# Kernel optimization log

Measured on AMD Instinct MI355X. Metric: run time of the kernel, lower is better.

## Reference

```python
import jax, jax.numpy as jnp
import numpy as np

NUM_PERS = 16
D = 128
N = 4096
EPSILON = 0.1
EPS_NORM = 1e-12  # matches torch F.normalize default eps


def setup_inputs() -> dict:
    key = jax.random.key(0)
    k1, k2 = jax.random.split(key)
    context = jax.random.normal(k1, (N, D), dtype=jnp.float32)
    # xavier_uniform for shape (num_pers, input_size): bound = sqrt(6/(fan_in+fan_out))
    bound = float(np.sqrt(6.0 / (NUM_PERS + D)))
    weight_tensor = jax.random.uniform(k2, (NUM_PERS, D), dtype=jnp.float32,
                                       minval=-bound, maxval=bound)
    return {"context": context, "weight_tensor": weight_tensor}


def reference(context, weight_tensor):
    # context: [N, D]; weight_tensor: [P, D]
    # per-perspective weighted features: [P, N, D]
    context_fc = context[None, :, :] * weight_tensor[:, None, :]
    # L2 normalize along feature dim (torch F.normalize: x / max(||x||, eps))
    norm = jnp.maximum(jnp.linalg.norm(context_fc, axis=-1, keepdims=True), EPS_NORM)
    context_norm = context_fc / norm
    # cosine similarity per perspective, mean over perspectives: [N, N]
    attention = jnp.einsum('pnd,pmd->pnm', context_norm, context_norm).mean(0)
    # epsilon neighbourhood with markoff_value = 0
    mask = (attention > EPSILON).astype(attention.dtype)
    return attention * mask
```

## Files before the change

kernel.cpp:

```cpp
#include <hip/hip_runtime.h>
#include <math.h>

#define N 4096
#define D 128
#define P 16
#define KK 2048
#define NT 32
#define NBLK (NT * (NT + 1) / 2)
#define LCAP 2048
#define CAP (1u << 20)
#define WIN 1.5e-3f
#define ZSCALE 256.0f
#define OSCALE (1.0f / 16777216.0f * 16.0f)

typedef _Float16 half_t;
typedef __attribute__((ext_vector_type(8))) _Float16 f16x8;
typedef __attribute__((ext_vector_type(4))) float f32x4;
typedef __attribute__((address_space(1))) const unsigned int* gptr_t;
typedef __attribute__((address_space(3))) unsigned int* lptr_t;

__global__ __launch_bounds__(256) void k_pack(const float* __restrict__ c,
                                              const float* __restrict__ w,
                                              double* __restrict__ rnorm,
                                              half_t* __restrict__ zb,
                                              unsigned* gcnt, unsigned* govf,
                                              int do_init) {
    int n = blockIdx.x, tid = threadIdx.x;
    if (do_init && n == 0 && tid == 0) { *gcnt = 0; *govf = 0; }
    int p = tid >> 4, d0 = (tid & 15) * 8;
    const float* cc = c + (size_t)n * D + d0;
    const float* ww = w + (size_t)p * D + d0;
    float cv[8], wv[8];
    *(float4*)&cv[0] = *(const float4*)&cc[0];
    *(float4*)&cv[4] = *(const float4*)&cc[4];
    *(float4*)&wv[0] = *(const float4*)&ww[0];
    *(float4*)&wv[4] = *(const float4*)&ww[4];
    double s = 0.0;
#pragma unroll
    for (int i = 0; i < 8; ++i) {
        double v = (double)cv[i] * (double)wv[i];
        s += v * v;
    }
#pragma unroll
    for (int o = 1; o < 16; o <<= 1) s += __shfl_xor(s, o, 64);
    double rn = 1.0 / fmax(sqrt(s), 1e-12);
    if ((tid & 15) == 0) rnorm[p * N + n] = rn;
    float rnf = (float)rn;
    f16x8 o8;
#pragma unroll
    for (int i = 0; i < 8; ++i) o8[i] = (half_t)(cv[i] * wv[i] * rnf * ZSCALE);
    *(f16x8*)&zb[(size_t)n * KK + tid * 8] = o8;
}

template <bool FUSED>
__global__ __launch_bounds__(256, 4) void k_gemm(const half_t* __restrict__ zb,
                                                 float* __restrict__ out,
                                                 unsigned* __restrict__ gcnt,
                                                 unsigned* __restrict__ govf,
                                                 unsigned* __restrict__ glist) {
    __shared__ __align__(16) half_t As[2][128 * 32];
    __shared__ __align__(16) half_t Bs[2][128 * 32];
    __shared__ unsigned lds_list[LCAP];
    __shared__ unsigned lds_cnt, lds_base, lds_tot;

    int tid = threadIdx.x;
    if (FUSED && tid == 0) lds_cnt = 0;

    int lane = tid & 63, wv = tid >> 6;
    int wr = wv >> 1, wc = wv & 1;

    int braw = blockIdx.x;
    int b = (braw & 7) * (NBLK / 8) + (braw >> 3);
    int ti = 0;
    while (b >= NT - ti) { b -= NT - ti; ++ti; }
    int tj = ti + b;
    int n0 = ti * 128, m0 = tj * 128;

    f32x4 acc[4][4] = {};
    int lrow = lane >> 2;
    int lchunk = (((lane & 3) ^ ((lrow >> 1) & 3)) * 8);

    auto STAGE = [&](int buf, int k0) {
#pragma unroll
        for (int h = 0; h < 2; ++h) {
            int s = h * 4 + wv;
            int row = s * 16 + lrow;
            __builtin_amdgcn_global_load_lds(
                (gptr_t)(zb + (size_t)(n0 + row) * KK + k0 + lchunk),
                (lptr_t)(&As[buf][s * 512]), 16, 0, 0);
            __builtin_amdgcn_global_load_lds(
                (gptr_t)(zb + (size_t)(m0 + row) * KK + k0 + lchunk),
                (lptr_t)(&Bs[buf][s * 512]), 16, 0, 0);
        }
    };

    int kk_c = lane >> 4;
    int rsel = lane & 15;
    int kphys = (kk_c ^ ((rsel >> 1) & 3)) * 8;

    auto COMPUTE = [&](int cur) {
        f16x8 af[4], bfr[4];
#pragma unroll
        for (int f = 0; f < 4; ++f) {
            af[f]  = *(f16x8*)&As[cur][(wr * 64 + f * 16 + rsel) * 32 + kphys];
            bfr[f] = *(f16x8*)&Bs[cur][(wc * 64 + f * 16 + rsel) * 32 + kphys];
        }
#pragma unroll
        for (int i = 0; i < 4; ++i)
#pragma unroll
            for (int j = 0; j < 4; ++j)
                acc[i][j] = __builtin_amdgcn_mfma_f32_16x16x32_f16(af[i], bfr[j], acc[i][j], 0, 0, 0);
    };

    STAGE(0, 0);

#pragma unroll 2
    for (int t = 0; t < 63; ++t) {
        int cur = t & 1;
        STAGE(cur ^ 1, (t + 1) * 32);
        asm volatile("s_waitcnt vmcnt(4)" ::: "memory");
        __builtin_amdgcn_sched_barrier(0);
        __builtin_amdgcn_s_barrier();
        __builtin_amdgcn_sched_barrier(0);
        COMPUTE(cur);
        asm volatile("s_waitcnt lgkmcnt(0)" ::: "memory");
        __builtin_amdgcn_sched_barrier(0);
        __builtin_amdgcn_s_barrier();
        __builtin_amdgcn_sched_barrier(0);
    }
    asm volatile("s_waitcnt vmcnt(0)" ::: "memory");
    __builtin_amdgcn_sched_barrier(0);
    __builtin_amdgcn_s_barrier();
    __builtin_amdgcn_sched_barrier(0);
    COMPUTE(1);

    int colD = lane & 15, rq = lane >> 4;
    bool mir = (ti != tj);
#pragma unroll
    for (int i = 0; i < 4; ++i)
#pragma unroll
        for (int j = 0; j < 4; ++j) {
            int rbase = n0 + wr * 64 + i * 16 + rq * 4;
            int ccol = m0 + wc * 64 + j * 16 + colD;
            float4 mv;
#pragma unroll
            for (int q = 0; q < 4; ++q) {
                float a = acc[i][j][q] * OSCALE;
                float sv;
                if (FUSED) {
                    bool flg = fabsf(a - 0.1f) < WIN;
                    sv = flg ? a : (a > 0.1f ? a : 0.0f);
                    if (flg) {
                        unsigned pos = atomicAdd(&lds_cnt, 1u);
                        unsigned ent = (unsigned)(rbase + q) | ((unsigned)ccol << 12) |
                                       (mir ? (1u << 24) : 0u);
                        if (pos < LCAP) lds_list[pos] = ent;
                    }
                } else {
                    sv = a;
                }
                out[(size_t)(rbase + q) * N + ccol] = sv;
                ((float*)&mv)[q] = sv;
            }
            if (mir) *(float4*)&out[(size_t)ccol * N + rbase] = mv;
        }

    if (FUSED) {
        __syncthreads();
        if (tid == 0) {
            unsigned tot = lds_cnt;
            unsigned cnt = tot > LCAP ? LCAP : tot;
            lds_tot = cnt;
            lds_base = atomicAdd(gcnt, cnt);
            if (tot > LCAP) atomicOr(govf, 1u);
        }
        __syncthreads();
        unsigned cnt = lds_tot, base = lds_base;
        for (unsigned e = tid; e < cnt; e += 256) {
            unsigned gi = base + e;
            if (gi < CAP) glist[gi] = lds_list[e];
            else atomicOr(govf, 1u);
        }
    }
}

__global__ __launch_bounds__(256) void k_fix3(const float* __restrict__ c,
                                              const float* __restrict__ w,
                                              const double* __restrict__ rnorm,
                                              const unsigned* __restrict__ gcnt,
                                              const unsigned* __restrict__ govf,
                                              const unsigned* __restrict__ glist,
                                              float* __restrict__ out) {
    __shared__ double w2[D * P];
    for (int e = threadIdx.x; e < P * D; e += 256) {
        int p = e >> 7, d = e & 127;
        double wv = (double)w[p * D + d];
        w2[d * P + p] = wv * wv;
    }
    __syncthreads();

    if (*govf) {
        size_t stride = (size_t)gridDim.x * 256;
        for (size_t idx = (size_t)blockIdx.x * 256 + threadIdx.x; idx < (size_t)N * N;
             idx += stride) {
            float a = out[idx];
            if (fabsf(a - 0.1f) >= WIN) {
                out[idx] = (a > 0.1f) ? a : 0.0f;
                continue;
            }
            int n = (int)(idx >> 12), m = (int)(idx & (N - 1));
            const float* cn = c + (size_t)n * D;
            const float* cm = c + (size_t)m * D;
            double acc[P];
#pragma unroll
            for (int p = 0; p < P; ++p) acc[p] = 0.0;
            for (int d0 = 0; d0 < D; d0 += 4) {
                float4 a4 = *(const float4*)&cn[d0];
                float4 b4 = *(const float4*)&cm[d0];
                float av[4] = {a4.x, a4.y, a4.z, a4.w};
                float bv[4] = {b4.x, b4.y, b4.z, b4.w};
#pragma unroll
                for (int q = 0; q < 4; ++q) {
                    double pr = (double)av[q] * (double)bv[q];
#pragma unroll
                    for (int p = 0; p < P; ++p) acc[p] += pr * w2[(d0 + q) * P + p];
                }
            }
            double t = 0.0;
#pragma unroll
            for (int p = 0; p < P; ++p)
                t += acc[p] * (rnorm[p * N + n] * rnorm[p * N + m]);
            double fin = t * 0.0625;
            out[idx] = (fin > 0.1) ? (float)fin : 0.0f;
        }
        return;
    }

    unsigned count = *gcnt;
    if (count > CAP) count = CAP;
    unsigned stride = gridDim.x * 256;
    for (unsigned e = blockIdx.x * 256 + threadIdx.x; e < count; e += stride) {
        unsigned u = glist[e];
        int n = u & 4095, m = (u >> 12) & 4095;
        const float* cn = c + (size_t)n * D;
        const float* cm = c + (size_t)m * D;
        double acc[P];
#pragma unroll
        for (int p = 0; p < P; ++p) acc[p] = 0.0;
        for (int d0 = 0; d0 < D; d0 += 4) {
            float4 a4 = *(const float4*)&cn[d0];
            float4 b4 = *(const float4*)&cm[d0];
            float av[4] = {a4.x, a4.y, a4.z, a4.w};
            float bv[4] = {b4.x, b4.y, b4.z, b4.w};
#pragma unroll
            for (int q = 0; q < 4; ++q) {
                double pr = (double)av[q] * (double)bv[q];
#pragma unroll
                for (int p = 0; p < P; ++p) acc[p] += pr * w2[(d0 + q) * P + p];
            }
        }
        double t = 0.0;
#pragma unroll
        for (int p = 0; p < P; ++p)
            t += acc[p] * (rnorm[p * N + n] * rnorm[p * N + m]);
        double fin = t * 0.0625;
        float res = (fin > 0.1) ? (float)fin : 0.0f;
        out[(size_t)n * N + m] = res;
        if (u >> 24) out[(size_t)m * N + n] = res;
    }
}

__global__ __launch_bounds__(256) void k_fix_full(const float* __restrict__ c,
                                                  const float* __restrict__ w,
                                                  const double* __restrict__ rnorm,
                                                  float* __restrict__ out) {
    __shared__ double w2[D * P];
    for (int e = threadIdx.x; e < P * D; e += 256) {
        int p = e >> 7, d = e & 127;
        double wv = (double)w[p * D + d];
        w2[d * P + p] = wv * wv;
    }
    __syncthreads();
    size_t stride = (size_t)gridDim.x * 256;
    for (size_t idx = (size_t)blockIdx.x * 256 + threadIdx.x; idx < (size_t)N * N;
         idx += stride) {
        float a = out[idx];
        if (fabsf(a - 0.1f) >= WIN) {
            out[idx] = (a > 0.1f) ? a : 0.0f;
            continue;
        }
        int n = (int)(idx >> 12), m = (int)(idx & (N - 1));
        const float* cn = c + (size_t)n * D;
        const float* cm = c + (size_t)m * D;
        double acc[P];
#pragma unroll
        for (int p = 0; p < P; ++p) acc[p] = 0.0;
        for (int d0 = 0; d0 < D; d0 += 4) {
            float4 a4 = *(const float4*)&cn[d0];
            float4 b4 = *(const float4*)&cm[d0];
            float av[4] = {a4.x, a4.y, a4.z, a4.w};
            float bv[4] = {b4.x, b4.y, b4.z, b4.w};
#pragma unroll
            for (int q = 0; q < 4; ++q) {
                double pr = (double)av[q] * (double)bv[q];
#pragma unroll
                for (int p = 0; p < P; ++p) acc[p] += pr * w2[(d0 + q) * P + p];
            }
        }
        double t = 0.0;
#pragma unroll
        for (int p = 0; p < P; ++p)
            t += acc[p] * (rnorm[p * N + n] * rnorm[p * N + m]);
        double fin = t * 0.0625;
        out[idx] = (fin > 0.1) ? (float)fin : 0.0f;
    }
}

extern "C" void kernel_launch(void* const* d_in, const int* in_sizes, int n_in,
                              void* d_out, int out_size, void* d_ws, size_t ws_size,
                              hipStream_t stream) {
    const float* c = (const float*)d_in[0];
    const float* w = (const float*)d_in[1];
    float* out = (float*)d_out;
    char* ws = (char*)d_ws;

    double* rnorm = (double*)ws;
    size_t off = (size_t)P * N * 8;
    unsigned* gcnt = (unsigned*)(ws + off);
    unsigned* govf = gcnt + 1;
    unsigned* glist = (unsigned*)(ws + off + 128);
    half_t* zb = (half_t*)(ws + off + 128 + (size_t)CAP * 4);
    size_t need = off + 128 + (size_t)CAP * 4 + (size_t)N * KK * 2;

    if (ws_size >= need) {
        k_pack<<<N, 256, 0, stream>>>(c, w, rnorm, zb, gcnt, govf, 1);
        k_gemm<true><<<NBLK, 256, 0, stream>>>(zb, out, gcnt, govf, glist);
        k_fix3<<<512, 256, 0, stream>>>(c, w, rnorm, gcnt, govf, glist, out);
    } else {
        half_t* zb2 = (half_t*)(ws + off);
        k_pack<<<N, 256, 0, stream>>>(c, w, rnorm, zb2, nullptr, nullptr, 0);
        k_gemm<false><<<NBLK, 256, 0, stream>>>(zb2, out, nullptr, nullptr, nullptr);
        k_fix_full<<<4096, 256, 0, stream>>>(c, w, rnorm, out);
    }
}
```

Before: 95.63 us.

## Double GEMM K-tile depth to 64 with XOR swizzled LDS layout

The K tile of the main GEMM grows from 32 to 64 halves, which halves the number of main-loop iterations and barrier pairs. Global-to-LDS staging is rewritten to copy full 128-byte rows using an XOR swizzle by row index, and the fragment reads use the matching swizzle. The doubled LDS footprint forces launch bounds down to 2 blocks per SIMD group, trading occupancy for fewer synchronisations and more MFMA work between barriers.

```diff
diff --git a/kernel.cpp b/kernel.cpp
--- a/kernel.cpp
+++ b/kernel.cpp
@@ -53,13 +53,13 @@
 }
 
 template <bool FUSED>
-__global__ __launch_bounds__(256, 4) void k_gemm(const half_t* __restrict__ zb,
+__global__ __launch_bounds__(256, 2) void k_gemm(const half_t* __restrict__ zb,
                                                  float* __restrict__ out,
                                                  unsigned* __restrict__ gcnt,
                                                  unsigned* __restrict__ govf,
                                                  unsigned* __restrict__ glist) {
-    __shared__ __align__(16) half_t As[2][128 * 32];
-    __shared__ __align__(16) half_t Bs[2][128 * 32];
+    __shared__ __align__(16) half_t As[2][128 * 64];
+    __shared__ __align__(16) half_t Bs[2][128 * 64];
     __shared__ unsigned lds_list[LCAP];
     __shared__ unsigned lds_cnt, lds_base, lds_tot;
 
@@ -77,48 +77,55 @@
     int n0 = ti * 128, m0 = tj * 128;
 
     f32x4 acc[4][4] = {};
-    int lrow = lane >> 2;
-    int lchunk = (((lane & 3) ^ ((lrow >> 1) & 3)) * 8);
-
-    auto STAGE = [&](int buf, int k0) {
-#pragma unroll
-        for (int h = 0; h < 2; ++h) {
-            int s = h * 4 + wv;
-            int row = s * 16 + lrow;
+
+    auto STAGE = [&](int buf, int kt) {
+        int k0 = kt * 64;
+#pragma unroll
+        for (int i = 0; i < 4; ++i) {
+            int piece = i * 256 + tid;
+            int r = piece >> 3, sl = piece & 7;
+            int cch = sl ^ (r & 7);
             __builtin_amdgcn_global_load_lds(
-                (gptr_t)(zb + (size_t)(n0 + row) * KK + k0 + lchunk),
-                (lptr_t)(&As[buf][s * 512]), 16, 0, 0);
+                (gptr_t)(zb + (size_t)(n0 + r) * KK + k0 + cch * 8),
+                (lptr_t)(&As[buf][piece * 8]), 16, 0, 0);
             __builtin_amdgcn_global_load_lds(
-                (gptr_t)(zb + (size_t)(m0 + row) * KK + k0 + lchunk),
-                (lptr_t)(&Bs[buf][s * 512]), 16, 0, 0);
+                (gptr_t)(zb + (size_t)(m0 + r) * KK + k0 + cch * 8),
+                (lptr_t)(&Bs[buf][piece * 8]), 16, 0, 0);
         }
     };
 
-    int kk_c = lane >> 4;
-    int rsel = lane & 15;
-    int kphys = (kk_c ^ ((rsel >> 1) & 3)) * 8;
+    int rsel = lane & 15, kk_c = lane >> 4;
 
     auto COMPUTE = [&](int cur) {
-        f16x8 af[4], bfr[4];
-#pragma unroll
-        for (int f = 0; f < 4; ++f) {
-            af[f]  = *(f16x8*)&As[cur][(wr * 64 + f * 16 + rsel) * 32 + kphys];
-            bfr[f] = *(f16x8*)&Bs[cur][(wc * 64 + f * 16 + rsel) * 32 + kphys];
-        }
-#pragma unroll
-        for (int i = 0; i < 4; ++i)
-#pragma unroll
-            for (int j = 0; j < 4; ++j)
-                acc[i][j] = __builtin_amdgcn_mfma_f32_16x16x32_f16(af[i], bfr[j], acc[i][j], 0, 0, 0);
+        f16x8 af[2][4], bfr[2][4];
+#pragma unroll
+        for (int kh = 0; kh < 2; ++kh) {
+            int c = kh * 4 + kk_c;
+#pragma unroll
+            for (int f = 0; f < 4; ++f) {
+                int ra = wr * 64 + f * 16 + rsel;
+                af[kh][f] = *(const f16x8*)&As[cur][ra * 64 + (c ^ (ra & 7)) * 8];
+                int rb = wc * 64 + f * 16 + rsel;
+                bfr[kh][f] = *(const f16x8*)&Bs[cur][rb * 64 + (c ^ (rb & 7)) * 8];
+            }
+        }
+#pragma unroll
+        for (int kh = 0; kh < 2; ++kh)
+#pragma unroll
+            for (int i = 0; i < 4; ++i)
+#pragma unroll
+                for (int j = 0; j < 4; ++j)
+                    acc[i][j] = __builtin_amdgcn_mfma_f32_16x16x32_f16(
+                        af[kh][i], bfr[kh][j], acc[i][j], 0, 0, 0);
     };
 
     STAGE(0, 0);
 
 #pragma unroll 2
-    for (int t = 0; t < 63; ++t) {
+    for (int t = 0; t < 31; ++t) {
         int cur = t & 1;
-        STAGE(cur ^ 1, (t + 1) * 32);
-        asm volatile("s_waitcnt vmcnt(4)" ::: "memory");
+        STAGE(cur ^ 1, t + 1);
+        asm volatile("s_waitcnt vmcnt(8)" ::: "memory");
         __builtin_amdgcn_sched_barrier(0);
         __builtin_amdgcn_s_barrier();
         __builtin_amdgcn_sched_barrier(0);
```

Result: slower. 105.8 us (+10.7%).
